# Optimization experiments

Hardware: AMD Instinct MI355X
Metric: run time of the kernel (lower is better)

Reference implementation:

```python
import jax, jax.numpy as jnp
import numpy as np

HASHMAP_SIZES = [65536, 262144]
HASHMAP_DIM = 4
RESO = 2097152
OUTPUT_DIM = 48


def setup_inputs() -> dict:
    key = jax.random.key(0)
    k1, k2, k3, k4 = jax.random.split(key, 4)
    total = sum(HASHMAP_SIZES)
    # codes initialized uniform(-1, 1) as in torch.nn.init.uniform_
    codes = jax.random.uniform(k1, (total, HASHMAP_DIM), dtype=jnp.float32, minval=-1.0, maxval=1.0)
    # bias-free linear head: stored as [in, out] so forward is feats @ W
    fan_in = len(HASHMAP_SIZES) * HASHMAP_DIM
    W = jax.random.normal(k2, (fan_in, OUTPUT_DIM), dtype=jnp.float32) / np.sqrt(fan_in)
    map_65536 = jax.random.randint(k3, (RESO, HASHMAP_DIM), 0, 65536, dtype=jnp.int64) if jax.config.jax_enable_x64 else jax.random.randint(k3, (RESO, HASHMAP_DIM), 0, 65536, dtype=jnp.int32)
    map_262144 = jax.random.randint(k4, (RESO, HASHMAP_DIM), 0, 262144, dtype=jnp.int32)
    return {"codes": codes, "W": W, "map_65536": map_65536, "map_262144": map_262144}


def _gather_level(code, idx_map):
    # code: [size, dim]; idx_map: [reso, dim]; out[n, i] = code[idx_map[n, i], i]
    dim_idx = jnp.arange(code.shape[1])[None, :]  # [1, dim]
    return code[idx_map, dim_idx]  # [reso, dim]


def reference(codes, W, map_65536, map_262144):
    # split stacked codebook into per-level tables
    code0 = codes[: HASHMAP_SIZES[0]]                      # [65536, 4]
    code1 = codes[HASHMAP_SIZES[0] : HASHMAP_SIZES[0] + HASHMAP_SIZES[1]]  # [262144, 4]
    out0 = _gather_level(code0, map_65536)    # [RESO, 4]
    out1 = _gather_level(code1, map_262144)   # [RESO, 4]
    feats = jnp.concatenate([out0, out1], axis=1)  # [RESO, 8]
    return feats @ W  # [RESO, 48]
```

## Files before the change

### kernel.cpp

```cpp
#include <hip/hip_runtime.h>


#define RESO    2097152
#define OUT_DIM 48
#define LVL0    65536
#define LVL1    262144
#define NCODES  (LVL0 + LVL1)
#define BLK     192
#define TILE    256
#define NITER   16

typedef int            vi4 __attribute__((ext_vector_type(4)));
typedef float          vf4 __attribute__((ext_vector_type(4)));
typedef unsigned short vu4 __attribute__((ext_vector_type(4)));

static __device__ __forceinline__ unsigned short f2bf_rne(float x) {
    unsigned int u = __float_as_uint(x);
    u += 0x7fffu + ((u >> 16) & 1u);
    return (unsigned short)(u >> 16);
}
static __device__ __forceinline__ float bf2f(unsigned short h) {
    return __uint_as_float(((unsigned int)h) << 16);
}

__global__ __launch_bounds__(256) void convert_kernel(
    const float* __restrict__ codes, unsigned short* __restrict__ bf)
{
    const int i = blockIdx.x * 256 + threadIdx.x;
    const vf4 v = ((const vf4*)codes)[i];
    vu4 o;
    o.x = f2bf_rne(v.x); o.y = f2bf_rne(v.y);
    o.z = f2bf_rne(v.z); o.w = f2bf_rne(v.w);
    ((vu4*)bf)[i] = o;
}

__global__ __launch_bounds__(BLK) void gshash_bf16_kernel(
    const unsigned short* __restrict__ tab,
    const float* __restrict__ W,
    const vi4*   __restrict__ map0,
    const vi4*   __restrict__ map1,
    float*       __restrict__ out)
{
    __shared__ float feats[TILE * 8];

    const int t     = threadIdx.x;
    const int col4  = t % 12;
    const int rbase = t / 12;
    const size_t row0 = (size_t)blockIdx.x * TILE;

    vf4 Wv[8];
    #pragma unroll
    for (int k = 0; k < 8; ++k)
        Wv[k] = ((const vf4*)(W + k * OUT_DIM))[col4];

    const unsigned short* __restrict__ t1 = tab + LVL0 * 4;

    #pragma unroll
    for (int half = 0; half < 2; ++half) {
        const int r = half * BLK + t;
        if (half == 0 || t < TILE - BLK) {
            const vi4 m0 = __builtin_nontemporal_load(&map0[row0 + r]);
            const vi4 m1 = __builtin_nontemporal_load(&map1[row0 + r]);
            vf4 a, b;
            a.x = bf2f(tab[m0.x * 4 + 0]);
            a.y = bf2f(tab[m0.y * 4 + 1]);
            a.z = bf2f(tab[m0.z * 4 + 2]);
            a.w = bf2f(tab[m0.w * 4 + 3]);
            b.x = bf2f(t1[m1.x * 4 + 0]);
            b.y = bf2f(t1[m1.y * 4 + 1]);
            b.z = bf2f(t1[m1.z * 4 + 2]);
            b.w = bf2f(t1[m1.w * 4 + 3]);
            *(vf4*)&feats[r * 8]     = a;
            *(vf4*)&feats[r * 8 + 4] = b;
        }
    }

    __syncthreads();

    vf4* __restrict__ out4 = (vf4*)(out + row0 * OUT_DIM);

    #pragma unroll
    for (int j = 0; j < NITER; ++j) {
        const int r = j * 16 + rbase;
        const vf4 fa = *(const vf4*)&feats[r * 8];
        const vf4 fb = *(const vf4*)&feats[r * 8 + 4];

        vf4 acc = fa.x * Wv[0];
        acc += fa.y * Wv[1];
        acc += fa.z * Wv[2];
        acc += fa.w * Wv[3];
        acc += fb.x * Wv[4];
        acc += fb.y * Wv[5];
        acc += fb.z * Wv[6];
        acc += fb.w * Wv[7];

        __builtin_nontemporal_store(acc, &out4[j * BLK + t]);
    }
}

__global__ __launch_bounds__(BLK) void gshash_f32_kernel(
    const float* __restrict__ codes,
    const float* __restrict__ W,
    const vi4*   __restrict__ map0,
    const vi4*   __restrict__ map1,
    float*       __restrict__ out)
{
    __shared__ float feats[TILE * 8];
    const int t     = threadIdx.x;
    const int col4  = t % 12;
    const int rbase = t / 12;
    const size_t row0 = (size_t)blockIdx.x * TILE;

    vf4 Wv[8];
    #pragma unroll
    for (int k = 0; k < 8; ++k)
        Wv[k] = ((const vf4*)(W + k * OUT_DIM))[col4];

    const float* __restrict__ c1 = codes + LVL0 * 4;

    #pragma unroll
    for (int half = 0; half < 2; ++half) {
        const int r = half * BLK + t;
        if (half == 0 || t < TILE - BLK) {
            const vi4 m0 = __builtin_nontemporal_load(&map0[row0 + r]);
            const vi4 m1 = __builtin_nontemporal_load(&map1[row0 + r]);
            vf4 a, b;
            a.x = codes[m0.x * 4 + 0];
            a.y = codes[m0.y * 4 + 1];
            a.z = codes[m0.z * 4 + 2];
            a.w = codes[m0.w * 4 + 3];
            b.x = c1[m1.x * 4 + 0];
            b.y = c1[m1.y * 4 + 1];
            b.z = c1[m1.z * 4 + 2];
            b.w = c1[m1.w * 4 + 3];
            *(vf4*)&feats[r * 8]     = a;
            *(vf4*)&feats[r * 8 + 4] = b;
        }
    }
    __syncthreads();

    vf4* __restrict__ out4 = (vf4*)(out + row0 * OUT_DIM);
    #pragma unroll
    for (int j = 0; j < NITER; ++j) {
        const int r = j * 16 + rbase;
        const vf4 fa = *(const vf4*)&feats[r * 8];
        const vf4 fb = *(const vf4*)&feats[r * 8 + 4];
        vf4 acc = fa.x * Wv[0];
        acc += fa.y * Wv[1];
        acc += fa.z * Wv[2];
        acc += fa.w * Wv[3];
        acc += fb.x * Wv[4];
        acc += fb.y * Wv[5];
        acc += fb.z * Wv[6];
        acc += fb.w * Wv[7];
        __builtin_nontemporal_store(acc, &out4[j * BLK + t]);
    }
}

extern "C" void kernel_launch(void* const* d_in, const int* in_sizes, int n_in,
                              void* d_out, int out_size, void* d_ws, size_t ws_size,
                              hipStream_t stream) {
    const float* codes = (const float*)d_in[0];
    const float* W     = (const float*)d_in[1];
    const vi4*   map0  = (const vi4*)d_in[2];
    const vi4*   map1  = (const vi4*)d_in[3];
    float*       out   = (float*)d_out;

    const size_t tab_bytes = (size_t)NCODES * 4 * sizeof(unsigned short);
    const int    grid      = RESO / TILE;

    if (ws_size >= tab_bytes) {
        unsigned short* tab = (unsigned short*)d_ws;
        convert_kernel<<<NCODES / 256, 256, 0, stream>>>(codes, tab);
        gshash_bf16_kernel<<<grid, BLK, 0, stream>>>(tab, W, map0, map1, out);
    } else {
        gshash_f32_kernel<<<grid, BLK, 0, stream>>>(codes, W, map0, map1, out);
    }
}
```

Before: 164.8 us.

## Warp-specialize bf16 kernel into producer/consumer pipeline with LDS ring buffer

Replaces the one-tile-per-block bf16 kernel with a persistent-style block of 320 threads. Two producer wavefronts prefetch maps and gather codebook entries for 16 tiles into a 4-slot LDS ring. Three consumer wavefronts run the 8x48 matvec and stream out results, with the two sides synchronised through spin-waited LDS counters. The aim is to overlap random-gather latency with output stores. In exchange it cuts the grid 16-fold, leaving far fewer blocks to hide latency, and adds spin-wait and occupancy risk.

Measured after the change: 161.7 us. No clear change (-1.9%).

```diff
diff --git a/kernel.cpp b/kernel.cpp
--- a/kernel.cpp
+++ b/kernel.cpp
@@ -4,11 +4,14 @@
 #define RESO    2097152
 #define OUT_DIM 48
 #define LVL0    65536
-#define LVL1    262144
-#define NCODES  (LVL0 + LVL1)
-#define BLK     192
+#define NCODES  327680
+#define BLK     320
+#define NCONS   192
 #define TILE    256
 #define NITER   16
+#define TPB     16
+#define NSLOT   4
+#define NBLK    (RESO / (TILE * TPB))
 
 typedef int            vi4 __attribute__((ext_vector_type(4)));
 typedef float          vf4 __attribute__((ext_vector_type(4)));
@@ -34,71 +37,126 @@
     ((vu4*)bf)[i] = o;
 }
 
-__global__ __launch_bounds__(BLK) void gshash_bf16_kernel(
+__global__ __launch_bounds__(BLK) void gshash_pc_kernel(
     const unsigned short* __restrict__ tab,
     const float* __restrict__ W,
     const vi4*   __restrict__ map0,
     const vi4*   __restrict__ map1,
     float*       __restrict__ out)
 {
-    __shared__ float feats[TILE * 8];
-
-    const int t     = threadIdx.x;
-    const int col4  = t % 12;
-    const int rbase = t / 12;
-    const size_t row0 = (size_t)blockIdx.x * TILE;
-
-    vf4 Wv[8];
-    #pragma unroll
-    for (int k = 0; k < 8; ++k)
-        Wv[k] = ((const vf4*)(W + k * OUT_DIM))[col4];
-
-    const unsigned short* __restrict__ t1 = tab + LVL0 * 4;
-
-    #pragma unroll
-    for (int half = 0; half < 2; ++half) {
-        const int r = half * BLK + t;
-        if (half == 0 || t < TILE - BLK) {
-            const vi4 m0 = __builtin_nontemporal_load(&map0[row0 + r]);
-            const vi4 m1 = __builtin_nontemporal_load(&map1[row0 + r]);
-            vf4 a, b;
-            a.x = bf2f(tab[m0.x * 4 + 0]);
-            a.y = bf2f(tab[m0.y * 4 + 1]);
-            a.z = bf2f(tab[m0.z * 4 + 2]);
-            a.w = bf2f(tab[m0.w * 4 + 3]);
-            b.x = bf2f(t1[m1.x * 4 + 0]);
-            b.y = bf2f(t1[m1.y * 4 + 1]);
-            b.z = bf2f(t1[m1.z * 4 + 2]);
-            b.w = bf2f(t1[m1.w * 4 + 3]);
-            *(vf4*)&feats[r * 8]     = a;
-            *(vf4*)&feats[r * 8 + 4] = b;
-        }
-    }
-
+    __shared__ float feats[NSLOT][TILE * 8];
+    __shared__ int   pcnt[NSLOT];
+    __shared__ int   ccnt[NSLOT];
+
+    const int t = threadIdx.x;
+    if (t < NSLOT) { pcnt[t] = 0; ccnt[t] = 0; }
     __syncthreads();
 
-    vf4* __restrict__ out4 = (vf4*)(out + row0 * OUT_DIM);
-
-    #pragma unroll
-    for (int j = 0; j < NITER; ++j) {
-        const int r = j * 16 + rbase;
-        const vf4 fa = *(const vf4*)&feats[r * 8];
-        const vf4 fb = *(const vf4*)&feats[r * 8 + 4];
-
-        vf4 acc = fa.x * Wv[0];
-        acc += fa.y * Wv[1];
-        acc += fa.z * Wv[2];
-        acc += fa.w * Wv[3];
-        acc += fb.x * Wv[4];
-        acc += fb.y * Wv[5];
-        acc += fb.z * Wv[6];
-        acc += fb.w * Wv[7];
-
-        __builtin_nontemporal_store(acc, &out4[j * BLK + t]);
-    }
-}
-
-__global__ __launch_bounds__(BLK) void gshash_f32_kernel(
+    const size_t row00 = (size_t)blockIdx.x * (TPB * TILE);
+    volatile int* vp = pcnt;
+    volatile int* vc = ccnt;
+
+    if (t >= NCONS) {
+        const int p = t - NCONS;
+        const unsigned short* __restrict__ t1 = tab + LVL0 * 4;
+        const bool lane0 = ((t & 63) == 0);
+
+        vi4 MA0, MA1, NA0, NA1, MB0, MB1, NB0, NB1;
+        unsigned short gA[16], gB[16];
+
+        #define PMAPS(j, M0, M1, N0, N1) {                                   \
+            const size_t r0 = row00 + (size_t)(j) * TILE;                    \
+            M0 = __builtin_nontemporal_load(&map0[r0 + p]);                  \
+            M1 = __builtin_nontemporal_load(&map1[r0 + p]);                  \
+            N0 = __builtin_nontemporal_load(&map0[r0 + 128 + p]);            \
+            N1 = __builtin_nontemporal_load(&map1[r0 + 128 + p]);            \
+        }
+        #define PGATH(M0, M1, N0, N1, G) {                                   \
+            G[0]  = tab[M0.x * 4 + 0];  G[1]  = tab[M0.y * 4 + 1];           \
+            G[2]  = tab[M0.z * 4 + 2];  G[3]  = tab[M0.w * 4 + 3];           \
+            G[4]  = t1[M1.x * 4 + 0];   G[5]  = t1[M1.y * 4 + 1];            \
+            G[6]  = t1[M1.z * 4 + 2];   G[7]  = t1[M1.w * 4 + 3];            \
+            G[8]  = tab[N0.x * 4 + 0];  G[9]  = tab[N0.y * 4 + 1];           \
+            G[10] = tab[N0.z * 4 + 2];  G[11] = tab[N0.w * 4 + 3];           \
+            G[12] = t1[N1.x * 4 + 0];   G[13] = t1[N1.y * 4 + 1];            \
+            G[14] = t1[N1.z * 4 + 2];   G[15] = t1[N1.w * 4 + 3];            \
+        }
+        #define PWRITE(G, s) {                                               \
+            vf4 a, b, c, d;                                                  \
+            a.x = bf2f(G[0]);  a.y = bf2f(G[1]);  a.z = bf2f(G[2]);  a.w = bf2f(G[3]);  \
+            b.x = bf2f(G[4]);  b.y = bf2f(G[5]);  b.z = bf2f(G[6]);  b.w = bf2f(G[7]);  \
+            c.x = bf2f(G[8]);  c.y = bf2f(G[9]);  c.z = bf2f(G[10]); c.w = bf2f(G[11]); \
+            d.x = bf2f(G[12]); d.y = bf2f(G[13]); d.z = bf2f(G[14]); d.w = bf2f(G[15]); \
+            *(vf4*)&feats[s][p * 8]             = a;                         \
+            *(vf4*)&feats[s][p * 8 + 4]         = b;                         \
+            *(vf4*)&feats[s][(128 + p) * 8]     = c;                         \
+            *(vf4*)&feats[s][(128 + p) * 8 + 4] = d;                         \
+        }
+
+        PMAPS(0, MA0, MA1, NA0, NA1);
+        PGATH(MA0, MA1, NA0, NA1, gA);
+        PMAPS(1, MB0, MB1, NB0, NB1);
+
+        #pragma unroll
+        for (int i = 0; i < TPB; ++i) {
+            const int s = i & (NSLOT - 1);
+            const int k = i >> 2;
+            if ((i & 1) == 0) {
+                if (i + 1 < TPB) PGATH(MB0, MB1, NB0, NB1, gB);
+                if (i + 2 < TPB) PMAPS(i + 2, MA0, MA1, NA0, NA1);
+                while (vc[s] < 3 * k) __builtin_amdgcn_s_sleep(1);
+                asm volatile("" ::: "memory");
+                PWRITE(gA, s);
+            } else {
+                if (i + 1 < TPB) PGATH(MA0, MA1, NA0, NA1, gA);
+                if (i + 2 < TPB) PMAPS(i + 2, MB0, MB1, NB0, NB1);
+                while (vc[s] < 3 * k) __builtin_amdgcn_s_sleep(1);
+                asm volatile("" ::: "memory");
+                PWRITE(gB, s);
+            }
+            asm volatile("s_waitcnt lgkmcnt(0)" ::: "memory");
+            if (lane0) atomicAdd(&pcnt[s], 1);
+        }
+        #undef PMAPS
+        #undef PGATH
+        #undef PWRITE
+    } else {
+        const int col4  = t % 12;
+        const int rbase = t / 12;
+        vf4 Wv[8];
+        #pragma unroll
+        for (int w = 0; w < 8; ++w)
+            Wv[w] = ((const vf4*)(W + w * OUT_DIM))[col4];
+
+        for (int i = 0; i < TPB; ++i) {
+            const int s = i & (NSLOT - 1);
+            const int k = i >> 2;
+            while (vp[s] < 2 * (k + 1)) __builtin_amdgcn_s_sleep(1);
+            asm volatile("" ::: "memory");
+
+            vf4* __restrict__ out4 = (vf4*)(out + (row00 + (size_t)i * TILE) * OUT_DIM);
+            #pragma unroll
+            for (int j = 0; j < NITER; ++j) {
+                const int r = j * 16 + rbase;
+                const vf4 fa = *(const vf4*)&feats[s][r * 8];
+                const vf4 fb = *(const vf4*)&feats[s][r * 8 + 4];
+                vf4 acc = fa.x * Wv[0];
+                acc += fa.y * Wv[1];
+                acc += fa.z * Wv[2];
+                acc += fa.w * Wv[3];
+                acc += fb.x * Wv[4];
+                acc += fb.y * Wv[5];
+                acc += fb.z * Wv[6];
+                acc += fb.w * Wv[7];
+                __builtin_nontemporal_store(acc, &out4[j * NCONS + t]);
+            }
+            asm volatile("s_waitcnt lgkmcnt(0)" ::: "memory");
+            if ((t & 63) == 0) atomicAdd(&ccnt[s], 1);
+        }
+    }
+}
+
+__global__ __launch_bounds__(192) void gshash_f32_kernel(
     const float* __restrict__ codes,
     const float* __restrict__ W,
     const vi4*   __restrict__ map0,
@@ -113,15 +171,14 @@
 
     vf4 Wv[8];
     #pragma unroll
-    for (int k = 0; k < 8; ++k)
-        Wv[k] = ((const vf4*)(W + k * OUT_DIM))[col4];
+    for (int w = 0; w < 8; ++w)
+        Wv[w] = ((const vf4*)(W + w * OUT_DIM))[col4];
 
     const float* __restrict__ c1 = codes + LVL0 * 4;
-
     #pragma unroll
     for (int half = 0; half < 2; ++half) {
-        const int r = half * BLK + t;
-        if (half == 0 || t < TILE - BLK) {
+        const int r = half * 192 + t;
+        if (half == 0 || t < TILE - 192) {
             const vi4 m0 = __builtin_nontemporal_load(&map0[row0 + r]);
             const vi4 m1 = __builtin_nontemporal_load(&map1[row0 + r]);
             vf4 a, b;
@@ -153,7 +210,7 @@
         acc += fb.y * Wv[5];
         acc += fb.z * Wv[6];
         acc += fb.w * Wv[7];
-        __builtin_nontemporal_store(acc, &out4[j * BLK + t]);
+        __builtin_nontemporal_store(acc, &out4[j * 192 + t]);
     }
 }
 
@@ -167,13 +224,12 @@
     float*       out   = (float*)d_out;
 
     const size_t tab_bytes = (size_t)NCODES * 4 * sizeof(unsigned short);
-    const int    grid      = RESO / TILE;
 
     if (ws_size >= tab_bytes) {
         unsigned short* tab = (unsigned short*)d_ws;
         convert_kernel<<<NCODES / 256, 256, 0, stream>>>(codes, tab);
-        gshash_bf16_kernel<<<grid, BLK, 0, stream>>>(tab, W, map0, map1, out);
+        gshash_pc_kernel<<<NBLK, BLK, 0, stream>>>(tab, W, map0, map1, out);
     } else {
-        gshash_f32_kernel<<<grid, BLK, 0, stream>>>(codes, W, map0, map1, out);
-    }
-}
+        gshash_f32_kernel<<<RESO / TILE, 192, 0, stream>>>(codes, W, map0, map1, out);
+    }
+}
```
